# Optimization experiments

Hardware: AMD Instinct MI355X
Metric: run time of the kernel (lower is better)

## Reference

```python
import jax, jax.numpy as jnp
import numpy as np

EMBED_DIM = 1024
NUM_HEADS = 16
HEAD_DIM = EMBED_DIM // NUM_HEADS


def setup_inputs() -> dict:
    key = jax.random.key(0)
    k1, k2, k3, k4 = jax.random.split(key, 4)
    B, N, C = 4, 4096, EMBED_DIM
    x = jax.random.normal(k1, (B, N, C), dtype=jnp.float32)
    scale = 1.0 / np.sqrt(C)
    W_qkv = jax.random.normal(k2, (C, 3 * C), dtype=jnp.float32) * scale
    W_out = jax.random.normal(k3, (C, C), dtype=jnp.float32) * scale
    b_out = jax.random.normal(k4, (C,), dtype=jnp.float32) * 0.01
    return {"x": x, "W_qkv": W_qkv, "W_out": W_out, "b_out": b_out}


def reference(x, W_qkv, W_out, b_out):
    B, N, C = x.shape
    H, D = NUM_HEADS, HEAD_DIM
    qkv = (x @ W_qkv).reshape(B, N, 3, H, D)
    qkv = jnp.transpose(qkv, (2, 0, 3, 1, 4))  # (3, B, H, N, D)
    q, k, v = qkv[0], qkv[1], qkv[2]
    q = jax.nn.elu(q) + 1.0
    k = jax.nn.elu(k) + 1.0
    kv = jnp.einsum('bhnd,bhne->bhde', k, v)          # (B,H,D,D)
    num = jnp.einsum('bhnd,bhde->bhne', q, kv)        # (B,H,N,D)
    normalizer = jnp.einsum('bhnd,bhd->bhn', q, k.sum(axis=2))
    out = num / (normalizer[..., None] + 1e-6)
    out = jnp.transpose(out, (0, 2, 1, 3)).reshape(B, N, C)
    return out @ W_out + b_out
```

## Files before the change

### kernel.cpp

```cpp
#include <hip/hip_runtime.h>
#include <hip/hip_bf16.h>

using bf16x8 = __bf16 __attribute__((ext_vector_type(8)));
using f32x4  = float  __attribute__((ext_vector_type(4)));
using u16x8  = unsigned short __attribute__((ext_vector_type(8)));
using u16x4  = unsigned short __attribute__((ext_vector_type(4)));

__device__ __forceinline__ unsigned short f2bf(float f) {
  unsigned u = __builtin_bit_cast(unsigned, f);
  u += 0x7fffu + ((u >> 16) & 1u);
  return (unsigned short)(u >> 16);
}
__device__ __forceinline__ float bf2f(unsigned short h) {
  return __builtin_bit_cast(float, (unsigned)h << 16);
}

__device__ __forceinline__ void gload16(const void* g, void* l) {
  __builtin_amdgcn_global_load_lds(
      (const __attribute__((address_space(1))) void*)g,
      (__attribute__((address_space(3))) void*)l, 16, 0, 0);
}

__device__ __forceinline__ void barrier_raw() {
  asm volatile("" ::: "memory");
  __builtin_amdgcn_s_barrier();
  asm volatile("" ::: "memory");
}
#define LGKM0() asm volatile("s_waitcnt lgkmcnt(0)" ::: "memory")
#define LGKM8() asm volatile("s_waitcnt lgkmcnt(8)" ::: "memory")
#define VMC6()  asm volatile("s_waitcnt vmcnt(6)" ::: "memory")
#define VMC0()  asm volatile("s_waitcnt vmcnt(0)" ::: "memory")

__global__ __launch_bounds__(256) void prep_kernel(
    const float* __restrict__ x, unsigned short* __restrict__ xbf,
    const float* __restrict__ Wqkv, unsigned short* __restrict__ wqkvT,
    const float* __restrict__ Wout, unsigned short* __restrict__ woutT) {
  __shared__ float t[64][65];
  const int bid = blockIdx.x;
  if (bid < 2048) {
    int stride = 2048 * 256 * 8;
    for (int i = (bid * 256 + threadIdx.x) * 8; i < 16777216; i += stride) {
      float4 v0 = *reinterpret_cast<const float4*>(x + i);
      float4 v1 = *reinterpret_cast<const float4*>(x + i + 4);
      u16x8 o = { f2bf(v0.x), f2bf(v0.y), f2bf(v0.z), f2bf(v0.w),
                  f2bf(v1.x), f2bf(v1.y), f2bf(v1.z), f2bf(v1.w) };
      *reinterpret_cast<u16x8*>(xbf + i) = o;
    }
    return;
  }
  const float* in;
  unsigned short* out;
  int R, C, bx, by;
  if (bid < 2816) {
    in = Wqkv; out = wqkvT; R = 1024; C = 3072;
    bx = (bid - 2048) % 48; by = (bid - 2048) / 48;
  } else {
    in = Wout; out = woutT; R = 1024; C = 1024;
    bx = (bid - 2816) % 16; by = (bid - 2816) / 16;
  }
  int c0 = bx * 64, r0 = by * 64;
  int lx = threadIdx.x & 63, ly = threadIdx.x >> 6;
#pragma unroll
  for (int i = 0; i < 16; ++i) {
    int r = ly * 16 + i;
    t[r][lx] = in[(size_t)(r0 + r) * C + c0 + lx];
  }
  __syncthreads();
#pragma unroll
  for (int i = 0; i < 16; ++i) {
    int c = ly * 16 + i;
    out[(size_t)(c0 + c) * R + r0 + lx] = f2bf(t[lx][c]);
  }
}

__device__ __forceinline__ void gemm256_mainloop(
    const unsigned short* __restrict__ A, const unsigned short* __restrict__ Bt,
    int brow, int bcol, char* lds, f32x4 (&acc)[8][4]) {
  constexpr int NT = 16;
  const int tid  = threadIdx.x;
  const int lane = tid & 63;
  const int w    = tid >> 6;
  const int wr   = w >> 2, wc = w & 3;
  const int lr   = lane & 15, kg = lane >> 4;

  const int o0 = tid * 16;
  const int o1 = 8192 + tid * 16;
  const int p0 = o0 ^ (((o0 >> 7) & 7) << 4);
  const int p1 = o1 ^ (((o1 >> 7) & 7) << 4);
  const int off0 = (p0 >> 7) * 2048 + (p0 & 127);
  const int off1 = (p1 >> 7) * 2048 + (p1 & 127);
  const int wq = w << 10;

  const int xr  = (lr & 7) << 4;
  const int ck0 = (kg * 16) ^ xr;
  const int ck1 = (64 + kg * 16) ^ xr;
  const int aoff = wr * 16384 + lr * 128;
  const int boff = 32768 + (wc >> 1) * 16384 + (wc & 1) * 8192 + lr * 128;

  auto STAGE = [&](const unsigned short* G, int rowbase, int t, int region) {
    const char* gb = (const char*)(G + (size_t)rowbase * 1024 + t * 64);
    char* lb = lds + region + wq;
    gload16(gb + off0, lb);
    gload16(gb + off1, lb + 8192);
  };

  STAGE(Bt, bcol,       0, 32768);
  STAGE(Bt, bcol + 128, 0, 49152);
  STAGE(A,  brow,       0, 0);
  STAGE(A,  brow + 128, 0, 16384);
  STAGE(Bt, bcol,       1, 65536 + 32768);
  STAGE(Bt, bcol + 128, 1, 65536 + 49152);
  STAGE(A,  brow,       1, 65536);
  VMC6();
  barrier_raw();

  bf16x8 aF[4][2], bF[4][2];
  for (int t = 0; t < NT; ++t) {
    const int bufo  = (t & 1) << 16;
    const int nbufo = bufo ^ 65536;
    const char* LA = lds + bufo + aoff;
    const char* LB = lds + bufo + boff;

#pragma unroll
    for (int n = 0; n < 2; ++n) {
      bF[n][0] = __builtin_bit_cast(bf16x8, *(const u16x8*)(LB + n * 2048 + ck0));
      bF[n][1] = __builtin_bit_cast(bf16x8, *(const u16x8*)(LB + n * 2048 + ck1));
    }
#pragma unroll
    for (int m = 0; m < 4; ++m) {
      aF[m][0] = __builtin_bit_cast(bf16x8, *(const u16x8*)(LA + m * 2048 + ck0));
      aF[m][1] = __builtin_bit_cast(bf16x8, *(const u16x8*)(LA + m * 2048 + ck1));
    }
    if (t + 1 < NT) STAGE(A, brow + 128, t + 1, nbufo + 16384);
    LGKM8();
    barrier_raw();
    LGKM0();
    __builtin_amdgcn_s_setprio(1);
#pragma unroll
    for (int kk = 0; kk < 2; ++kk)
#pragma unroll
      for (int m = 0; m < 4; ++m)
#pragma unroll
        for (int n = 0; n < 2; ++n)
          acc[m][n] = __builtin_amdgcn_mfma_f32_16x16x32_bf16(aF[m][kk], bF[n][kk], acc[m][n], 0, 0, 0);
    __builtin_amdgcn_s_setprio(0);
    barrier_raw();

#pragma unroll
    for (int n = 2; n < 4; ++n) {
      bF[n][0] = __builtin_bit_cast(bf16x8, *(const u16x8*)(LB + n * 2048 + ck0));
      bF[n][1] = __builtin_bit_cast(bf16x8, *(const u16x8*)(LB + n * 2048 + ck1));
    }
    barrier_raw();
    LGKM0();
    __builtin_amdgcn_s_setprio(1);
#pragma unroll
    for (int kk = 0; kk < 2; ++kk)
#pragma unroll
      for (int m = 0; m < 4; ++m)
#pragma unroll
        for (int n = 2; n < 4; ++n)
          acc[m][n] = __builtin_amdgcn_mfma_f32_16x16x32_bf16(aF[m][kk], bF[n][kk], acc[m][n], 0, 0, 0);
    __builtin_amdgcn_s_setprio(0);
    barrier_raw();

#pragma unroll
    for (int m = 0; m < 4; ++m) {
      aF[m][0] = __builtin_bit_cast(bf16x8, *(const u16x8*)(LA + (m + 4) * 2048 + ck0));
      aF[m][1] = __builtin_bit_cast(bf16x8, *(const u16x8*)(LA + (m + 4) * 2048 + ck1));
    }
    if (t + 2 < NT) STAGE(Bt, bcol, t + 2, bufo + 32768);
    barrier_raw();
    LGKM0();
    __builtin_amdgcn_s_setprio(1);
#pragma unroll
    for (int kk = 0; kk < 2; ++kk)
#pragma unroll
      for (int m = 0; m < 4; ++m)
#pragma unroll
        for (int n = 2; n < 4; ++n)
          acc[m + 4][n] = __builtin_amdgcn_mfma_f32_16x16x32_bf16(aF[m][kk], bF[n][kk], acc[m + 4][n], 0, 0, 0);
    __builtin_amdgcn_s_setprio(0);
    barrier_raw();

    if (t + 2 < NT) {
      STAGE(Bt, bcol + 128, t + 2, bufo + 49152);
      STAGE(A,  brow,       t + 2, bufo);
    }
    barrier_raw();
    __builtin_amdgcn_s_setprio(1);
#pragma unroll
    for (int kk = 0; kk < 2; ++kk)
#pragma unroll
      for (int m = 0; m < 4; ++m)
#pragma unroll
        for (int n = 0; n < 2; ++n)
          acc[m + 4][n] = __builtin_amdgcn_mfma_f32_16x16x32_bf16(aF[m][kk], bF[n][kk], acc[m + 4][n], 0, 0, 0);
    __builtin_amdgcn_s_setprio(0);
    if (t + 2 < NT) { VMC6(); } else { VMC0(); }
    barrier_raw();
  }
}

__global__ __launch_bounds__(512, 2) void gemm_qkv(
    const unsigned short* __restrict__ xbf, const unsigned short* __restrict__ wt,
    unsigned short* __restrict__ q, unsigned short* __restrict__ k, unsigned short* __restrict__ v) {
  __shared__ __align__(16) char lds[131072];
  f32x4 acc[8][4] = {};
  const int bid = blockIdx.x;
  const int r = bid & 7, i = bid >> 3;
  const int tm = r * 8 + (i & 7);
  const int tn = i >> 3;
  const int brow = tm * 256, bcol = tn * 256;
  gemm256_mainloop(xbf, wt, brow, bcol, lds, acc);

  const int lane = threadIdx.x & 63, w = threadIdx.x >> 6;
  const int wr = w >> 2, wc = w & 3;
  const int lr = lane & 15, kg = lane >> 4;
#pragma unroll
  for (int m = 0; m < 8; ++m)
#pragma unroll
    for (int n = 0; n < 4; ++n)
#pragma unroll
      for (int rr = 0; rr < 4; ++rr) {
        int grow = brow + wr * 128 + m * 16 + kg * 4 + rr;
        int gcol = bcol + wc * 64 + n * 16 + lr;
        float val = acc[m][n][rr];
        int tt = gcol >> 10;
        int h = (gcol >> 6) & 15;
        int d = gcol & 63;
        int b = grow >> 12, s = grow & 4095;
        size_t idx = ((size_t)(b * 16 + h) * 4096 + s) * 64 + d;
        if (tt < 2) {
          val = val > 0.f ? val + 1.f : __expf(val);
          (tt == 0 ? q : k)[idx] = f2bf(val);
        } else {
          v[idx] = f2bf(val);
        }
      }
}

__global__ __launch_bounds__(512, 2) void gemm_out(
    const unsigned short* __restrict__ attn, const unsigned short* __restrict__ wt,
    const float* __restrict__ bias, float* __restrict__ out) {
  __shared__ __align__(16) char lds[131072];
  f32x4 acc[8][4] = {};
  const int bid = blockIdx.x;
  const int r = bid & 7, i = bid >> 3;
  const int tm = r * 8 + (i & 7);
  const int tn = i >> 3;
  const int brow = tm * 256, bcol = tn * 256;
  gemm256_mainloop(attn, wt, brow, bcol, lds, acc);

  const int lane = threadIdx.x & 63, w = threadIdx.x >> 6;
  const int wr = w >> 2, wc = w & 3;
  const int lr = lane & 15, kg = lane >> 4;
#pragma unroll
  for (int m = 0; m < 8; ++m)
#pragma unroll
    for (int n = 0; n < 4; ++n)
#pragma unroll
      for (int rr = 0; rr < 4; ++rr) {
        int grow = brow + wr * 128 + m * 16 + kg * 4 + rr;
        int gcol = bcol + wc * 64 + n * 16 + lr;
        out[(size_t)grow * 1024 + gcol] = acc[m][n][rr] + bias[gcol];
      }
}

__global__ __launch_bounds__(256) void kv_mfma(
    const unsigned short* __restrict__ k, const unsigned short* __restrict__ v,
    float* __restrict__ kv_part, float* __restrict__ ksum_part) {
  const int bid = blockIdx.x;
  const int bh = bid >> 1, half = bid & 1;
  const size_t nbase = (size_t)bh * 4096 + half * 2048;
  __shared__ unsigned short kt[64 * 72];
  __shared__ unsigned short vt[64 * 72];
  const int tid  = threadIdx.x;
  const int lane = tid & 63, w = tid >> 6;
  const int lr = lane & 15, kg = lane >> 4;
  const int srow = w * 16 + (lane >> 2);
  const int sd   = (lane & 3) * 16;

  f32x4 acc[4] = {{0.f,0.f,0.f,0.f},{0.f,0.f,0.f,0.f},{0.f,0.f,0.f,0.f},{0.f,0.f,0.f,0.f}};
  f32x4 ks[4]  = {{0.f,0.f,0.f,0.f},{0.f,0.f,0.f,0.f},{0.f,0.f,0.f,0.f},{0.f,0.f,0.f,0.f}};
  const u16x8 onesu = { 0x3F80,0x3F80,0x3F80,0x3F80,0x3F80,0x3F80,0x3F80,0x3F80 };
  const bf16x8 aone = __builtin_bit_cast(bf16x8, onesu);

  const int arow = w * 16 + lr;
  const int axor = ((arow >> 3) & 7) << 3;
  const unsigned short* aB[2];
  aB[0] = vt + arow * 72 + ((kg * 8) ^ axor);
  aB[1] = vt + arow * 72 + ((32 + kg * 8) ^ axor);
  const unsigned short* bB[4][2];
#pragma unroll
  for (int dt = 0; dt < 4; ++dt) {
    int drow = dt * 16 + lr;
    int dxor = ((drow >> 3) & 7) << 3;
    bB[dt][0] = kt + drow * 72 + ((kg * 8) ^ dxor);
    bB[dt][1] = kt + drow * 72 + ((32 + kg * 8) ^ dxor);
  }

  u16x8 pk0, pk1, pv0, pv1;
  auto LOADR = [&](int sub) {
    const unsigned short* kr = k + (nbase + (size_t)sub * 64 + srow) * 64 + sd;
    const unsigned short* vr = v + (nbase + (size_t)sub * 64 + srow) * 64 + sd;
    pk0 = *(const u16x8*)kr;  pk1 = *(const u16x8*)(kr + 8);
    pv0 = *(const u16x8*)vr;  pv1 = *(const u16x8*)(vr + 8);
  };
  LOADR(0);

  for (int sub = 0; sub < 32; ++sub) {
    __syncthreads();
    u16x8 k0 = pk0, k1 = pk1, v0 = pv0, v1 = pv1;
#pragma unroll
    for (int j = 0; j < 8; ++j) {
      int d0 = sd + j, d1 = sd + 8 + j;
      int x0 = ((d0 >> 3) & 7) << 3, x1 = ((d1 >> 3) & 7) << 3;
      kt[d0 * 72 + (srow ^ x0)] = k0[j];
      kt[d1 * 72 + (srow ^ x1)] = k1[j];
      vt[d0 * 72 + (srow ^ x0)] = v0[j];
      vt[d1 * 72 + (srow ^ x1)] = v1[j];
    }
    if (sub + 1 < 32) LOADR(sub + 1);
    __syncthreads();
#pragma unroll
    for (int kk = 0; kk < 2; ++kk) {
      bf16x8 af = __builtin_bit_cast(bf16x8, *(const u16x8*)aB[kk]);
#pragma unroll
      for (int dt = 0; dt < 4; ++dt) {
        bf16x8 bf = __builtin_bit_cast(bf16x8, *(const u16x8*)bB[dt][kk]);
        acc[dt] = __builtin_amdgcn_mfma_f32_16x16x32_bf16(af, bf, acc[dt], 0, 0, 0);
        if (w == 0)
          ks[dt] = __builtin_amdgcn_mfma_f32_16x16x32_bf16(aone, bf, ks[dt], 0, 0, 0);
      }
    }
  }

  float* kvp = kv_part + ((size_t)half * 128 + bh) * 4096;
#pragma unroll
  for (int dt = 0; dt < 4; ++dt)
#pragma unroll
    for (int r = 0; r < 4; ++r) {
      int e = w * 16 + kg * 4 + r;
      kvp[e * 64 + dt * 16 + lr] = acc[dt][r];
    }
  if (w == 0 && kg == 0) {
    float* ksp = ksum_part + (size_t)half * 8192 + bh * 64;
#pragma unroll
    for (int dt = 0; dt < 4; ++dt) ksp[dt * 16 + lr] = ks[dt][0];
  }
}

__global__ __launch_bounds__(256) void num_kernel(
    const unsigned short* __restrict__ q, const float* __restrict__ kv_part,
    const float* __restrict__ ksum_part, unsigned short* __restrict__ attn) {
  const int bid = blockIdx.x;
  const int bh = bid >> 6, sblk = bid & 63;
  const int b = bh >> 4, h = bh & 15;
  __shared__ unsigned short kvs[64 * 72];
  __shared__ float ksum_s[64];
  __shared__ float norm_s[64];
  const int tid = threadIdx.x;
  const float* kv0 = kv_part + (size_t)bh * 4096;
  const float* kv1 = kv_part + (size_t)(128 + bh) * 4096;
#pragma unroll
  for (int r = 0; r < 4; ++r) {
    int e = r * 1024 + tid * 4;
    float4 f0 = *reinterpret_cast<const float4*>(&kv0[e]);
    float4 f1 = *reinterpret_cast<const float4*>(&kv1[e]);
    float4 f = { f0.x + f1.x, f0.y + f1.y, f0.z + f1.z, f0.w + f1.w };
    int row = e >> 6, col = e & 63;
    u16x4 o = { f2bf(f.x), f2bf(f.y), f2bf(f.z), f2bf(f.w) };
    *reinterpret_cast<u16x4*>(&kvs[row * 72 + col]) = o;
  }
  if (tid < 16) {
    float4 f0 = *reinterpret_cast<const float4*>(&ksum_part[bh * 64 + tid * 4]);
    float4 f1 = *reinterpret_cast<const float4*>(&ksum_part[8192 + bh * 64 + tid * 4]);
    ksum_s[tid * 4 + 0] = f0.x + f1.x; ksum_s[tid * 4 + 1] = f0.y + f1.y;
    ksum_s[tid * 4 + 2] = f0.z + f1.z; ksum_s[tid * 4 + 3] = f0.w + f1.w;
  }
  __syncthreads();

  const int lane = tid & 63, w = tid >> 6;
  const int lr = lane & 15, kg = lane >> 4;
  const int s0 = sblk * 64 + w * 16;
  const unsigned short* qrow = q + ((size_t)bh * 4096 + s0 + lr) * 64 + kg * 8;
  u16x8 a0u = *reinterpret_cast<const u16x8*>(qrow);
  u16x8 a1u = *reinterpret_cast<const u16x8*>(qrow + 32);
  bf16x8 a0 = __builtin_bit_cast(bf16x8, a0u);
  bf16x8 a1 = __builtin_bit_cast(bf16x8, a1u);

  float p = 0.f;
#pragma unroll
  for (int j = 0; j < 8; ++j) {
    p += bf2f(a0u[j]) * ksum_s[kg * 8 + j];
    p += bf2f(a1u[j]) * ksum_s[32 + kg * 8 + j];
  }
  p += __shfl_xor(p, 16);
  p += __shfl_xor(p, 32);
  if (kg == 0) norm_s[w * 16 + lr] = p;

  f32x4 accs[4];
#pragma unroll
  for (int jf = 0; jf < 4; ++jf) {
    u16x8 b0u = *reinterpret_cast<const u16x8*>(&kvs[(jf * 16 + lr) * 72 + kg * 8]);
    u16x8 b1u = *reinterpret_cast<const u16x8*>(&kvs[(jf * 16 + lr) * 72 + 32 + kg * 8]);
    f32x4 c = {0.f, 0.f, 0.f, 0.f};
    c = __builtin_amdgcn_mfma_f32_16x16x32_bf16(a0, __builtin_bit_cast(bf16x8, b0u), c, 0, 0, 0);
    c = __builtin_amdgcn_mfma_f32_16x16x32_bf16(a1, __builtin_bit_cast(bf16x8, b1u), c, 0, 0, 0);
    accs[jf] = c;
  }
  float dn[4];
#pragma unroll
  for (int r = 0; r < 4; ++r) dn[r] = norm_s[w * 16 + kg * 4 + r] + 1e-6f;

  unsigned short* ab = attn + (size_t)b * 4096 * 1024 + h * 64;
#pragma unroll
  for (int jf = 0; jf < 4; ++jf)
#pragma unroll
    for (int r = 0; r < 4; ++r) {
      int s = s0 + kg * 4 + r;
      int e2 = jf * 16 + lr;
      ab[(size_t)s * 1024 + e2] = f2bf(accs[jf][r] / dn[r]);
    }
}

extern "C" void kernel_launch(void* const* d_in, const int* in_sizes, int n_in,
                              void* d_out, int out_size, void* d_ws, size_t ws_size,
                              hipStream_t stream) {
  const float* x     = (const float*)d_in[0];
  const float* W_qkv = (const float*)d_in[1];
  const float* W_out = (const float*)d_in[2];
  const float* b_out = (const float*)d_in[3];
  float* out = (float*)d_out;

  unsigned short* xbf   = (unsigned short*)d_ws;
  unsigned short* attnb = xbf;
  unsigned short* wqkvT = xbf + 16777216;
  unsigned short* woutT = wqkvT + 3145728;
  unsigned short* qb    = woutT + 1048576;
  unsigned short* kb    = qb + 16777216;
  unsigned short* vb    = kb + 16777216;
  float* kvp            = (float*)(vb + 16777216);
  float* ksp            = kvp + 1048576;

  prep_kernel<<<3072, 256, 0, stream>>>(x, xbf, W_qkv, wqkvT, W_out, woutT);
  gemm_qkv<<<768, 512, 0, stream>>>(xbf, wqkvT, qb, kb, vb);
  kv_mfma<<<256, 256, 0, stream>>>(kb, vb, kvp, ksp);
  num_kernel<<<4096, 256, 0, stream>>>(qb, kvp, ksp, attnb);
  gemm_out<<<256, 512, 0, stream>>>(attnb, woutT, b_out, out);
}
```

Before: 230.5 us.

## Make QKV GEMM persistent over three column tiles with prefetched prologues

The QKV projection kernel now launches 256 blocks instead of 768, and each block walks three output column tiles in sequence. The shared-memory prologue loads for the next tile are issued before and after the current tile's epilogue, so global loads overlap with the ELU and scatter stores. The mainloop is split into prologue and body helpers, and the final-iteration wait is adjusted for this. The aim is to remove the partial second wave of the 768-block launch and hide pipeline fill, at the cost of only one block per CU instead of two co-resident blocks.

Result: slower. 393.3 us (+70.6%).

```diff
diff --git a/kernel.cpp b/kernel.cpp
--- a/kernel.cpp
+++ b/kernel.cpp
@@ -73,7 +73,49 @@
   }
 }
 
-__device__ __forceinline__ void gemm256_mainloop(
+__device__ __forceinline__ void gemm256_prologue_t0(
+    const unsigned short* __restrict__ A, const unsigned short* __restrict__ Bt,
+    int brow, int bcol, char* lds) {
+  const int tid = threadIdx.x;
+  const int o0 = tid * 16, o1 = 8192 + tid * 16;
+  const int p0 = o0 ^ (((o0 >> 7) & 7) << 4);
+  const int p1 = o1 ^ (((o1 >> 7) & 7) << 4);
+  const int off0 = (p0 >> 7) * 2048 + (p0 & 127);
+  const int off1 = (p1 >> 7) * 2048 + (p1 & 127);
+  const int wq = (tid >> 6) << 10;
+  auto STAGE = [&](const unsigned short* G, int rowbase, int region) {
+    const char* gb = (const char*)(G + (size_t)rowbase * 1024);
+    char* lb = lds + region + wq;
+    gload16(gb + off0, lb);
+    gload16(gb + off1, lb + 8192);
+  };
+  STAGE(Bt, bcol,       32768);
+  STAGE(Bt, bcol + 128, 49152);
+  STAGE(A,  brow,       0);
+  STAGE(A,  brow + 128, 16384);
+}
+__device__ __forceinline__ void gemm256_prologue_t1(
+    const unsigned short* __restrict__ A, const unsigned short* __restrict__ Bt,
+    int brow, int bcol, char* lds) {
+  const int tid = threadIdx.x;
+  const int o0 = tid * 16, o1 = 8192 + tid * 16;
+  const int p0 = o0 ^ (((o0 >> 7) & 7) << 4);
+  const int p1 = o1 ^ (((o1 >> 7) & 7) << 4);
+  const int off0 = (p0 >> 7) * 2048 + (p0 & 127);
+  const int off1 = (p1 >> 7) * 2048 + (p1 & 127);
+  const int wq = (tid >> 6) << 10;
+  auto STAGE = [&](const unsigned short* G, int rowbase, int region) {
+    const char* gb = (const char*)(G + (size_t)rowbase * 1024 + 64);
+    char* lb = lds + region + wq;
+    gload16(gb + off0, lb);
+    gload16(gb + off1, lb + 8192);
+  };
+  STAGE(Bt, bcol,       65536 + 32768);
+  STAGE(Bt, bcol + 128, 65536 + 49152);
+  STAGE(A,  brow,       65536);
+}
+
+__device__ __forceinline__ void gemm256_body(
     const unsigned short* __restrict__ A, const unsigned short* __restrict__ Bt,
     int brow, int bcol, char* lds, f32x4 (&acc)[8][4]) {
   constexpr int NT = 16;
@@ -104,16 +146,6 @@
     gload16(gb + off1, lb + 8192);
   };
 
-  STAGE(Bt, bcol,       0, 32768);
-  STAGE(Bt, bcol + 128, 0, 49152);
-  STAGE(A,  brow,       0, 0);
-  STAGE(A,  brow + 128, 0, 16384);
-  STAGE(Bt, bcol,       1, 65536 + 32768);
-  STAGE(Bt, bcol + 128, 1, 65536 + 49152);
-  STAGE(A,  brow,       1, 65536);
-  VMC6();
-  barrier_raw();
-
   bf16x8 aF[4][2], bF[4][2];
   for (int t = 0; t < NT; ++t) {
     const int bufo  = (t & 1) << 16;
@@ -197,7 +229,7 @@
         for (int n = 0; n < 2; ++n)
           acc[m + 4][n] = __builtin_amdgcn_mfma_f32_16x16x32_bf16(aF[m][kk], bF[n][kk], acc[m + 4][n], 0, 0, 0);
     __builtin_amdgcn_s_setprio(0);
-    if (t + 2 < NT) { VMC6(); } else { VMC0(); }
+    if (t + 2 < NT) { VMC6(); } else if (t + 1 < NT) { VMC0(); }
     barrier_raw();
   }
 }
@@ -210,34 +242,57 @@
   const int bid = blockIdx.x;
   const int r = bid & 7, i = bid >> 3;
   const int tm = r * 8 + (i & 7);
-  const int tn = i >> 3;
-  const int brow = tm * 256, bcol = tn * 256;
-  gemm256_mainloop(xbf, wt, brow, bcol, lds, acc);
+  const int tn0 = i >> 3;
+  const int brow = tm * 256;
 
   const int lane = threadIdx.x & 63, w = threadIdx.x >> 6;
   const int wr = w >> 2, wc = w & 3;
   const int lr = lane & 15, kg = lane >> 4;
-#pragma unroll
-  for (int m = 0; m < 8; ++m)
-#pragma unroll
-    for (int n = 0; n < 4; ++n)
-#pragma unroll
-      for (int rr = 0; rr < 4; ++rr) {
-        int grow = brow + wr * 128 + m * 16 + kg * 4 + rr;
-        int gcol = bcol + wc * 64 + n * 16 + lr;
-        float val = acc[m][n][rr];
-        int tt = gcol >> 10;
-        int h = (gcol >> 6) & 15;
-        int d = gcol & 63;
-        int b = grow >> 12, s = grow & 4095;
-        size_t idx = ((size_t)(b * 16 + h) * 4096 + s) * 64 + d;
-        if (tt < 2) {
-          val = val > 0.f ? val + 1.f : __expf(val);
-          (tt == 0 ? q : k)[idx] = f2bf(val);
-        } else {
-          v[idx] = f2bf(val);
+
+  gemm256_prologue_t0(xbf, wt, brow, tn0 * 256, lds);
+  gemm256_prologue_t1(xbf, wt, brow, tn0 * 256, lds);
+  VMC6();
+  barrier_raw();
+
+  for (int rep = 0; rep < 3; ++rep) {
+    const int bcol = (tn0 + rep * 4) * 256;
+    gemm256_body(xbf, wt, brow, bcol, lds, acc);
+
+    if (rep < 2) gemm256_prologue_t0(xbf, wt, brow, bcol + 1024, lds);
+
+#pragma unroll
+    for (int m = 0; m < 8; ++m)
+#pragma unroll
+      for (int n = 0; n < 4; ++n)
+#pragma unroll
+        for (int rr = 0; rr < 4; ++rr) {
+          int grow = brow + wr * 128 + m * 16 + kg * 4 + rr;
+          int gcol = bcol + wc * 64 + n * 16 + lr;
+          float val = acc[m][n][rr];
+          int tt = gcol >> 10;
+          int h = (gcol >> 6) & 15;
+          int d = gcol & 63;
+          int b = grow >> 12, s = grow & 4095;
+          size_t idx = ((size_t)(b * 16 + h) * 4096 + s) * 64 + d;
+          if (tt < 2) {
+            val = val > 0.f ? val + 1.f : __expf(val);
+            (tt == 0 ? q : k)[idx] = f2bf(val);
+          } else {
+            v[idx] = f2bf(val);
+          }
         }
-      }
+
+    if (rep < 2) {
+      gemm256_prologue_t1(xbf, wt, brow, bcol + 1024, lds);
+      VMC6();
+      barrier_raw();
+#pragma unroll
+      for (int m = 0; m < 8; ++m)
+#pragma unroll
+        for (int n = 0; n < 4; ++n)
+          acc[m][n] = f32x4{0.f, 0.f, 0.f, 0.f};
+    }
+  }
 }
 
 __global__ __launch_bounds__(512, 2) void gemm_out(
@@ -250,7 +305,12 @@
   const int tm = r * 8 + (i & 7);
   const int tn = i >> 3;
   const int brow = tm * 256, bcol = tn * 256;
-  gemm256_mainloop(attn, wt, brow, bcol, lds, acc);
+
+  gemm256_prologue_t0(attn, wt, brow, bcol, lds);
+  gemm256_prologue_t1(attn, wt, brow, bcol, lds);
+  VMC6();
+  barrier_raw();
+  gemm256_body(attn, wt, brow, bcol, lds, acc);
 
   const int lane = threadIdx.x & 63, w = threadIdx.x >> 6;
   const int wr = w >> 2, wc = w & 3;
@@ -445,7 +505,7 @@
   float* ksp            = kvp + 1048576;
 
   prep_kernel<<<3072, 256, 0, stream>>>(x, xbf, W_qkv, wqkvT, W_out, woutT);
-  gemm_qkv<<<768, 512, 0, stream>>>(xbf, wqkvT, qb, kb, vb);
+  gemm_qkv<<<256, 512, 0, stream>>>(xbf, wqkvT, qb, kb, vb);
   kv_mfma<<<256, 256, 0, stream>>>(kb, vb, kvp, ksp);
   num_kernel<<<4096, 256, 0, stream>>>(qb, kvp, ksp, attnb);
   gemm_out<<<256, 512, 0, stream>>>(attnb, woutT, b_out, out);
```
